# Optimization experiments

Hardware: AMD Instinct MI355X
Metric: run time of the kernel (lower is better)

Reference implementation:

```python
import jax, jax.numpy as jnp
import numpy as np

D_MODEL = 512
N_HEADS = 8
D_KV = 64
INNER = N_HEADS * D_KV
NUM_BUCKETS = 32
MAX_DISTANCE = 128
LN_EPS = 1e-6


def _relative_position_bucket(rel, num_buckets=NUM_BUCKETS, max_distance=MAX_DISTANCE):
    # bidirectional T5 bucketing
    nb = num_buckets // 2
    buckets = (rel > 0).astype(jnp.int32) * nb
    rel = jnp.abs(rel)
    max_exact = nb // 2
    is_small = rel < max_exact
    relf = jnp.maximum(rel.astype(jnp.float32), 1.0)  # guard log(0)
    large = max_exact + (
        jnp.log(relf / max_exact) / np.log(max_distance / max_exact) * (nb - max_exact)
    ).astype(jnp.int32)
    large = jnp.minimum(large, nb - 1)
    return buckets + jnp.where(is_small, rel, large)


def t5_layer_norm(x, weight, eps=LN_EPS):
    # T5 LayerNorm: no mean subtraction, no bias
    var = jnp.mean(jnp.square(x), axis=-1, keepdims=True)
    return x * jax.lax.rsqrt(var + eps) * weight


def compute_position_bias(rel_bias_table, q_len, k_len):
    ctx = jnp.arange(q_len)[:, None]
    mem = jnp.arange(k_len)[None, :]
    buckets = _relative_position_bucket(mem - ctx)  # [q, k]
    bias = rel_bias_table[buckets]                  # [q, k, H]
    return jnp.transpose(bias, (2, 0, 1))[None]     # [1, H, q, k]


def setup_inputs() -> dict:
    key = jax.random.key(0)
    ks = jax.random.split(key, 8)
    N, S = 8, 2048
    s = 1.0 / np.sqrt(D_MODEL)
    return {
        "hidden_states": jax.random.normal(ks[0], (N, S, D_MODEL), jnp.float32),
        "ln_weight": jnp.ones((D_MODEL,), jnp.float32),
        "wq": jax.random.normal(ks[1], (D_MODEL, INNER), jnp.float32) * s,
        "wk": jax.random.normal(ks[2], (D_MODEL, INNER), jnp.float32) * s,
        "wv": jax.random.normal(ks[3], (D_MODEL, INNER), jnp.float32) * s,
        "wo": jax.random.normal(ks[4], (INNER, D_MODEL), jnp.float32) * s,
        "rel_bias_table": jax.random.normal(ks[5], (NUM_BUCKETS, N_HEADS), jnp.float32) * 0.1,
        "seq_idx2graph_idx": jax.random.randint(ks[6], (8,), 0, 8, jnp.int64) if jax.config.jax_enable_x64 else jax.random.randint(ks[6], (8,), 0, 8, jnp.int32),
    }


def reference(hidden_states, ln_weight, wq, wk, wv, wo, rel_bias_table, seq_idx2graph_idx):
    N, S, _ = hidden_states.shape
    normed = t5_layer_norm(hidden_states, ln_weight)

    # T5Attention (no 1/sqrt(d) scaling in T5)
    q = jnp.einsum("nsd,de->nse", normed, wq).reshape(N, S, N_HEADS, D_KV)
    k = jnp.einsum("nsd,de->nse", normed, wk).reshape(N, S, N_HEADS, D_KV)
    v = jnp.einsum("nsd,de->nse", normed, wv).reshape(N, S, N_HEADS, D_KV)

    position_bias = compute_position_bias(rel_bias_table, S, S)  # [1,H,S,S]
    scores = jnp.einsum("nqhd,nkhd->nhqk", q, k) + position_bias
    attn = jax.nn.softmax(scores, axis=-1)
    ctx = jnp.einsum("nhqk,nkhd->nqhd", attn, v).reshape(N, S, INNER)
    attn_out = jnp.einsum("nse,ed->nsd", ctx, wo)

    # residual (dropout is identity in eval)
    hidden = hidden_states + attn_out
    remain_node_idx = jnp.arange(seq_idx2graph_idx.shape[0])
    return hidden, position_bias, remain_node_idx
```

## Files before the change

### kernel.cpp

```cpp
#include <hip/hip_runtime.h>
#include <hip/hip_bf16.h>
#include <math.h>

typedef __bf16 bf16;
typedef bf16 bf16x8 __attribute__((ext_vector_type(8)));
typedef bf16 bf16x4 __attribute__((ext_vector_type(4)));
typedef float f32x4 __attribute__((ext_vector_type(4)));
typedef float f32x16 __attribute__((ext_vector_type(16)));

#define MFMA16(a, b, c) __builtin_amdgcn_mfma_f32_16x16x32_bf16(a, b, c, 0, 0, 0)
#define MFMA32(a, b, c) __builtin_amdgcn_mfma_f32_32x32x16_bf16(a, b, c, 0, 0, 0)
#define LOG2E 1.4426950408889634f
#define NEG_SHIFT -40.0f

__device__ __forceinline__ void glds16(const bf16* g, bf16* l) {
  __builtin_amdgcn_global_load_lds(
      (const __attribute__((address_space(1))) void*)g,
      (__attribute__((address_space(3))) void*)l, 16, 0, 0);
}

__device__ inline unsigned pkbf(float a, float b) {
  union { bf16 h; unsigned short u; } ca, cb;
  ca.h = (bf16)a;
  cb.h = (bf16)b;
  return (unsigned)ca.u | ((unsigned)cb.u << 16);
}

__device__ inline float t5bias(const float* __restrict__ table, int h, int x) {
  if (x > 4094) return 0.f;
  int rel = x - 2047;
  int bucket = (rel > 0) ? 16 : 0;
  int ar = rel < 0 ? -rel : rel;
  int v;
  if (ar < 8) {
    v = ar;
  } else {
    double tt = log((double)ar / 8.0) / log(16.0) * 8.0;
    int lg = 8 + (int)tt;
    v = lg < 15 ? lg : 15;
  }
  return table[(bucket + v) * 8 + h];
}

__global__ __launch_bounds__(256) void prep_kernel(
    const float* __restrict__ hidden, const float* __restrict__ ln_w,
    const float* __restrict__ wq, const float* __restrict__ wk,
    const float* __restrict__ wv, const float* __restrict__ wo,
    const float* __restrict__ table, bf16* __restrict__ normed,
    float* __restrict__ lut, float4* __restrict__ lutq,
    float* __restrict__ out_remain, bf16* __restrict__ wt_qkv,
    bf16* __restrict__ wt_o) {
  __shared__ float tile[32][33];
  int bid = blockIdx.x;
  int t = threadIdx.x;
  if (bid < 4096) {
    int row = bid * 4 + (t >> 6);
    int lane = t & 63;
    const float4* xr = (const float4*)(hidden + (size_t)row * 512);
    float4 a = xr[lane];
    float4 b = xr[lane + 64];
    float s = a.x * a.x + a.y * a.y + a.z * a.z + a.w * a.w +
              b.x * b.x + b.y * b.y + b.z * b.z + b.w * b.w;
#pragma unroll
    for (int off = 32; off > 0; off >>= 1) s += __shfl_down(s, off, 64);
    float tot = __shfl(s, 0, 64);
    float rscale = rsqrtf(tot * (1.0f / 512.0f) + 1e-6f);
    float4 w0 = *(const float4*)(ln_w + 4 * lane);
    float4 w1 = *(const float4*)(ln_w + 256 + 4 * lane);
    bf16x4 o0, o1;
    o0[0] = (bf16)(a.x * rscale * w0.x);
    o0[1] = (bf16)(a.y * rscale * w0.y);
    o0[2] = (bf16)(a.z * rscale * w0.z);
    o0[3] = (bf16)(a.w * rscale * w0.w);
    o1[0] = (bf16)(b.x * rscale * w1.x);
    o1[1] = (bf16)(b.y * rscale * w1.y);
    o1[2] = (bf16)(b.z * rscale * w1.z);
    o1[3] = (bf16)(b.w * rscale * w1.w);
    *(bf16x4*)(normed + (size_t)row * 512 + 4 * lane) = o0;
    *(bf16x4*)(normed + (size_t)row * 512 + 256 + 4 * lane) = o1;
  } else if (bid < 4224) {
    int i = (bid - 4096) * 256 + t;
    int h = i >> 12;
    int d = i & 4095;
    lut[(size_t)h * 4096 + d] = t5bias(table, h, d);
    if (i < 8) out_remain[i] = (float)i;
  } else if (bid < 5248) {
    int bid2 = bid - 4224;
    int mat = bid2 >> 8;
    int rem = bid2 & 255;
    int e0 = (rem & 15) * 32;
    int k0 = (rem >> 4) * 32;
    int tx = t & 31, ty = t >> 5;
    const float* W = (mat == 0) ? wq : (mat == 1) ? wk : (mat == 2) ? wv : wo;
#pragma unroll
    for (int j = 0; j < 32; j += 8)
      tile[ty + j][tx] = W[(size_t)(k0 + ty + j) * 512 + e0 + tx];
    __syncthreads();
    bf16* dst = (mat < 3) ? (wt_qkv + (size_t)mat * 512 * 512) : wt_o;
#pragma unroll
    for (int j = 0; j < 32; j += 8)
      dst[(size_t)(e0 + ty + j) * 512 + k0 + tx] = (bf16)tile[tx][ty + j];
  } else {
    int i = (bid - 5248) * 256 + t;
    int h = i >> 12;
    int d = i & 4095;
    float4 o;
    o.x = t5bias(table, h, d);
    o.y = t5bias(table, h, d + 1);
    o.z = t5bias(table, h, d + 2);
    o.w = t5bias(table, h, d + 3);
    lutq[(size_t)h * 4096 + d] = o;
  }
}

__global__ __launch_bounds__(256) void qkv_gemm(
    const bf16* __restrict__ normed, const bf16* __restrict__ wt,
    bf16* __restrict__ qb, bf16* __restrict__ kb, bf16* __restrict__ vtb) {
  __shared__ __align__(16) char smem[19456];
  bf16* As = (bf16*)smem;
  bf16* Bs = (bf16*)(smem + 8192);
  int t = threadIdx.x;
  int wave = t >> 6, lane = t & 63;
  int quad = lane >> 4, lc = lane & 15;
  int wm = wave >> 1, wn = wave & 1;
  int m0 = blockIdx.x * 128, n0 = blockIdx.y * 128;

  f32x4 acc[4][4];
#pragma unroll
  for (int i = 0; i < 4; i++)
#pragma unroll
    for (int j = 0; j < 4; j++) acc[i][j] = (f32x4){0.f, 0.f, 0.f, 0.f};

  int rw = lane >> 2;
  int c8 = (lane & 3) * 8;
  const bf16* gA = normed + (size_t)(m0 + wave * 32 + rw) * 512 + c8;
  const bf16* gB = wt + (size_t)(n0 + wave * 32 + rw) * 512 + c8;
  bf16* lA = As + wave * 1024;
  bf16* lB = Bs + wave * 1024;

  for (int kt = 0; kt < 16; ++kt) {
    int k0 = kt * 32;
    __syncthreads();
    glds16(gA + k0, lA);
    glds16(gA + 16 * 512 + k0, lA + 512);
    glds16(gB + k0, lB);
    glds16(gB + 16 * 512 + k0, lB + 512);
    __syncthreads();
    bf16x8 af[4], bfr[4];
#pragma unroll
    for (int i = 0; i < 4; i++)
      af[i] = *(const bf16x8*)&As[(wm * 64 + i * 16 + lc) * 32 + quad * 8];
#pragma unroll
    for (int j = 0; j < 4; j++)
      bfr[j] = *(const bf16x8*)&Bs[(wn * 64 + j * 16 + lc) * 32 + quad * 8];
#pragma unroll
    for (int i = 0; i < 4; i++)
#pragma unroll
      for (int j = 0; j < 4; j++)
        acc[i][j] = MFMA16(af[i], bfr[j], acc[i][j]);
  }

  __syncthreads();
  int mat = n0 >> 9;
  int e_base = (n0 & 511) + wn * 64;
  int hh = e_base >> 6;
  int grow0 = m0 + wm * 64;
  int nbi = grow0 >> 11, sbase = grow0 & 2047;

  if (mat == 2) {
    bf16* dv = vtb + ((size_t)(nbi * 8 + hh) * 64) * 2048;
#pragma unroll
    for (int i = 0; i < 4; i++) {
      int s = sbase + i * 16 + quad * 4;
#pragma unroll
      for (int j = 0; j < 4; j++) {
        int d = j * 16 + lc;
        bf16x4 o4;
#pragma unroll
        for (int r = 0; r < 4; r++) o4[r] = (bf16)acc[i][j][r];
        *(bf16x4*)(dv + (size_t)d * 2048 + s) = o4;
      }
    }
  } else {
    bf16* dst0 = (mat == 0) ? qb : kb;
    bf16* dst = dst0 + (((size_t)nbi * 8 + hh) * 2048 + sbase) * 64;
    bf16* Cw = (bf16*)smem + wave * 2432;
#pragma unroll
    for (int p = 0; p < 2; ++p) {
#pragma unroll
      for (int i2 = 0; i2 < 2; ++i2) {
#pragma unroll
        for (int j = 0; j < 4; ++j)
#pragma unroll
          for (int r = 0; r < 4; ++r)
            Cw[(i2 * 16 + quad * 4 + r) * 76 + j * 16 + lc] =
                (bf16)acc[2 * p + i2][j][r];
      }
#pragma unroll
      for (int c = 0; c < 4; ++c) {
        bf16x8 vch =
            *(const bf16x8*)&Cw[(c * 8 + (lane >> 3)) * 76 + (lane & 7) * 8];
        *(bf16x8*)(dst + (size_t)(p * 32 + c * 8 + (lane >> 3)) * 64 +
                   (lane & 7) * 8) = vch;
      }
    }
  }
}

__global__ __launch_bounds__(256, 3) void attn_bias_kernel(
    const bf16* __restrict__ qg, const bf16* __restrict__ kg,
    const bf16* __restrict__ vtg, const float4* __restrict__ lutq,
    const float* __restrict__ lutg, bf16* __restrict__ ctx,
    float* __restrict__ bias_out) {
  __shared__ bf16 Ks[64][72];
  __shared__ bf16 Vs[64][72];
  int t = threadIdx.x;

  if (blockIdx.x >= 1024) {
    size_t i = (((size_t)blockIdx.x - 1024) * 256 + t) * 4;
    int h = (int)(i >> 22);
    int q = (int)((i >> 11) & 2047);
    int k = (int)(i & 2047);
    const float* lh = lutg + (size_t)h * 4096 + (2047 - q);
    float4 v = {lh[k], lh[k + 1], lh[k + 2], lh[k + 3]};
    *(float4*)(bias_out + i) = v;
    return;
  }

  int id = blockIdx.x;
  int xcd = id & 7, slot = id >> 3;
  int bh = xcd * 8 + (slot >> 4);
  int qt = slot & 15;
  int n = bh >> 3, h = bh & 7;
  int q0 = qt * 128;

  int wave = t >> 6, lane = t & 63;
  int l31 = lane & 31, hi = lane >> 5;
  int q = q0 + wave * 32 + l31;

  const float4* bq = lutq + (size_t)h * 4096;
  int cbase = 2047 + 4 * hi - q;

  const bf16* qp = qg + ((size_t)bh * 2048 + q) * 64;
  bf16x8 Qf[4];
#pragma unroll
  for (int c = 0; c < 4; c++) Qf[c] = *(const bf16x8*)(qp + c * 16 + hi * 8);

  f32x16 O[2];
#pragma unroll
  for (int i = 0; i < 2; i++)
#pragma unroll
    for (int e = 0; e < 16; e++) O[i][e] = 0.f;
  float lsum0 = 0.f, lsum1 = 0.f;

  int srow = t >> 2, scol = (t & 3) * 16;
  const bf16* kp = kg + (size_t)bh * 2048 * 64;
  const bf16* vp = vtg + (size_t)bh * 64 * 2048;

  bf16x8 kv0 = *(const bf16x8*)(kp + (size_t)srow * 64 + scol);
  bf16x8 kv1 = *(const bf16x8*)(kp + (size_t)srow * 64 + scol + 8);
  bf16x8 vv0 = *(const bf16x8*)(vp + (size_t)srow * 2048 + scol);
  bf16x8 vv1 = *(const bf16x8*)(vp + (size_t)srow * 2048 + scol + 8);

  for (int kt = 0; kt < 32; ++kt) {
    int kr0 = kt * 64;
    __syncthreads();
    *(bf16x8*)&Ks[srow][scol] = kv0;
    *(bf16x8*)&Ks[srow][scol + 8] = kv1;
    *(bf16x8*)&Vs[srow][scol] = vv0;
    *(bf16x8*)&Vs[srow][scol + 8] = vv1;
    __syncthreads();

    f32x16 st[2];
#pragma unroll
    for (int mi = 0; mi < 2; mi++)
#pragma unroll
      for (int g = 0; g < 4; g++) {
        float4 b4 = bq[cbase + kr0 + mi * 32 + 8 * g];
        st[mi][4 * g + 0] = b4.x;
        st[mi][4 * g + 1] = b4.y;
        st[mi][4 * g + 2] = b4.z;
        st[mi][4 * g + 3] = b4.w;
      }

    if (kt + 1 < 32) {
      int kn = kr0 + 64;
      kv0 = *(const bf16x8*)(kp + (size_t)(kn + srow) * 64 + scol);
      kv1 = *(const bf16x8*)(kp + (size_t)(kn + srow) * 64 + scol + 8);
      vv0 = *(const bf16x8*)(vp + (size_t)srow * 2048 + kn + scol);
      vv1 = *(const bf16x8*)(vp + (size_t)srow * 2048 + kn + scol + 8);
    }

#pragma unroll
    for (int mi = 0; mi < 2; mi++) {
#pragma unroll
      for (int c = 0; c < 4; c++) {
        bf16x8 kf = *(const bf16x8*)&Ks[mi * 32 + l31][c * 16 + hi * 8];
        st[mi] = MFMA32(kf, Qf[c], st[mi]);
      }
      unsigned D[8], X[8];
#pragma unroll
      for (int g = 0; g < 4; g++) {
#pragma unroll
        for (int e = 0; e < 4; e++) {
          float p = __builtin_amdgcn_exp2f(fmaf(st[mi][4 * g + e], LOG2E, NEG_SHIFT));
          st[mi][4 * g + e] = p;
          if (e & 1) lsum1 += p; else lsum0 += p;
        }
        D[2 * g] = pkbf(st[mi][4 * g + 0], st[mi][4 * g + 1]);
        D[2 * g + 1] = pkbf(st[mi][4 * g + 2], st[mi][4 * g + 3]);
      }
#pragma unroll
      for (int tt = 0; tt < 8; tt++) X[tt] = __shfl_xor(D[tt], 32, 64);

#pragma unroll
      for (int kk = 0; kk < 2; kk++) {
        int kc = 2 * mi + kk;
        int b = 4 * kk;
        unsigned f0 = hi ? X[b + 2] : D[b + 0];
        unsigned f1 = hi ? X[b + 3] : D[b + 1];
        unsigned f2 = hi ? D[b + 2] : X[b + 0];
        unsigned f3 = hi ? D[b + 3] : X[b + 1];
        union { uint4 u; bf16x8 v; } cv;
        cv.u = make_uint4(f0, f1, f2, f3);
        bf16x8 pf = cv.v;
#pragma unroll
        for (int md = 0; md < 2; md++) {
          bf16x8 vf = *(const bf16x8*)&Vs[md * 32 + l31][kc * 16 + hi * 8];
          O[md] = MFMA32(vf, pf, O[md]);
        }
      }
    }
  }

  float l_run = lsum0 + lsum1;
  l_run += __shfl_xor(l_run, 32, 64);
  float inv = 1.0f / l_run;
  bf16* cp = ctx + ((size_t)n * 2048 + q) * 512 + h * 64;
#pragma unroll
  for (int md = 0; md < 2; md++)
#pragma unroll
    for (int g = 0; g < 4; g++) {
      bf16x4 o4;
#pragma unroll
      for (int e = 0; e < 4; e++) o4[e] = (bf16)(O[md][4 * g + e] * inv);
      *(bf16x4*)(cp + md * 32 + 8 * g + hi * 4) = o4;
    }
}

__global__ __launch_bounds__(256) void oproj_gemm(
    const bf16* __restrict__ ctx, const bf16* __restrict__ wt_o,
    const float* __restrict__ hidden, float* __restrict__ out) {
  __shared__ __align__(16) char smem[16384];
  bf16* As = (bf16*)smem;
  bf16* Bs = (bf16*)(smem + 8192);
  int t = threadIdx.x;
  int wave = t >> 6, lane = t & 63;
  int quad = lane >> 4, lc = lane & 15;
  int wm = wave >> 1, wn = wave & 1;
  int m0 = blockIdx.x * 128, n0 = blockIdx.y * 128;

  f32x4 acc[4][4];
#pragma unroll
  for (int i = 0; i < 4; i++)
#pragma unroll
    for (int j = 0; j < 4; j++) acc[i][j] = (f32x4){0.f, 0.f, 0.f, 0.f};

  int rw = lane >> 2;
  int c8 = (lane & 3) * 8;
  const bf16* gA = ctx + (size_t)(m0 + wave * 32 + rw) * 512 + c8;
  const bf16* gB = wt_o + (size_t)(n0 + wave * 32 + rw) * 512 + c8;
  bf16* lA = As + wave * 1024;
  bf16* lB = Bs + wave * 1024;

  for (int kt = 0; kt < 16; ++kt) {
    int k0 = kt * 32;
    __syncthreads();
    glds16(gA + k0, lA);
    glds16(gA + 16 * 512 + k0, lA + 512);
    glds16(gB + k0, lB);
    glds16(gB + 16 * 512 + k0, lB + 512);
    __syncthreads();
    bf16x8 af[4], bfr[4];
#pragma unroll
    for (int i = 0; i < 4; i++)
      af[i] = *(const bf16x8*)&As[(wm * 64 + i * 16 + lc) * 32 + quad * 8];
#pragma unroll
    for (int j = 0; j < 4; j++)
      bfr[j] = *(const bf16x8*)&Bs[(wn * 64 + j * 16 + lc) * 32 + quad * 8];
#pragma unroll
    for (int i = 0; i < 4; i++)
#pragma unroll
      for (int j = 0; j < 4; j++)
        acc[i][j] = MFMA16(af[i], bfr[j], acc[i][j]);
  }

#pragma unroll
  for (int i = 0; i < 4; i++) {
#pragma unroll
    for (int j = 0; j < 4; j++) {
#pragma unroll
      for (int r = 0; r < 4; r++) {
        int grow = m0 + wm * 64 + i * 16 + quad * 4 + r;
        int gcol = n0 + wn * 64 + j * 16 + lc;
        size_t idx = (size_t)grow * 512 + gcol;
        out[idx] = acc[i][j][r] + hidden[idx];
      }
    }
  }
}

extern "C" void kernel_launch(void* const* d_in, const int* in_sizes, int n_in,
                              void* d_out, int out_size, void* d_ws, size_t ws_size,
                              hipStream_t stream) {
  const float* hidden = (const float*)d_in[0];
  const float* ln_w = (const float*)d_in[1];
  const float* wq = (const float*)d_in[2];
  const float* wk = (const float*)d_in[3];
  const float* wv = (const float*)d_in[4];
  const float* wo = (const float*)d_in[5];
  const float* table = (const float*)d_in[6];

  float* out_hidden = (float*)d_out;
  float* out_bias = out_hidden + (size_t)8 * 2048 * 512;
  float* out_remain = out_bias + (size_t)8 * 2048 * 2048;

  char* ws = (char*)d_ws;
  bf16* normed = (bf16*)(ws + 0);
  float* lut = (float*)(ws + 16777216);
  float4* lutq = (float4*)(ws + 16908288);
  bf16* wt_qkv = (bf16*)(ws + 17432576);
  bf16* wt_o = (bf16*)(ws + 19005440);
  bf16* qb = (bf16*)(ws + 19529728);
  bf16* kb = qb + (size_t)8 * 8 * 2048 * 64;
  bf16* vtb = kb + (size_t)8 * 8 * 2048 * 64;
  bf16* ctx = normed;

  prep_kernel<<<dim3(5376), dim3(256), 0, stream>>>(
      hidden, ln_w, wq, wk, wv, wo, table, normed, lut, lutq, out_remain,
      wt_qkv, wt_o);
  qkv_gemm<<<dim3(128, 12), dim3(256), 0, stream>>>(normed, wt_qkv, qb, kb, vtb);
  attn_bias_kernel<<<dim3(1024 + 32768), dim3(256), 0, stream>>>(
      qb, kb, vtb, lutq, lut, ctx, out_bias);
  oproj_gemm<<<dim3(128, 4), dim3(256), 0, stream>>>(ctx, wt_o, hidden, out_hidden);
}
```

Before: 358.4 us.

## Double-buffer attention K/V via async global-to-LDS loads with XOR swizzle

The attention kernel now stages K and V tiles directly into LDS with global_load_lds into two alternating buffers, so the next tile streams in while the current one is consumed. This replaces register staging and drops one barrier per iteration. Shared-memory rows are XOR-swizzled to avoid bank conflicts, and occupancy is raised to 4 blocks per SM. The QKV and output-projection GEMMs move to a 64-wide K tile with the same swizzled LDS layout, halving the number of barriers, at the cost of more LDS and tighter register limits.

```diff
diff --git a/kernel.cpp b/kernel.cpp
--- a/kernel.cpp
+++ b/kernel.cpp
@@ -116,9 +116,8 @@
 __global__ __launch_bounds__(256) void qkv_gemm(
     const bf16* __restrict__ normed, const bf16* __restrict__ wt,
     bf16* __restrict__ qb, bf16* __restrict__ kb, bf16* __restrict__ vtb) {
-  __shared__ __align__(16) char smem[19456];
-  bf16* As = (bf16*)smem;
-  bf16* Bs = (bf16*)(smem + 8192);
+  __shared__ __align__(16) bf16 As[128 * 64];
+  __shared__ __align__(16) bf16 Bs[128 * 64];
   int t = threadIdx.x;
   int wave = t >> 6, lane = t & 63;
   int quad = lane >> 4, lc = lane & 15;
@@ -131,33 +130,39 @@
 #pragma unroll
     for (int j = 0; j < 4; j++) acc[i][j] = (f32x4){0.f, 0.f, 0.f, 0.f};
 
-  int rw = lane >> 2;
-  int c8 = (lane & 3) * 8;
-  const bf16* gA = normed + (size_t)(m0 + wave * 32 + rw) * 512 + c8;
-  const bf16* gB = wt + (size_t)(n0 + wave * 32 + rw) * 512 + c8;
-  bf16* lA = As + wave * 1024;
-  bf16* lB = Bs + wave * 1024;
-
-  for (int kt = 0; kt < 16; ++kt) {
-    int k0 = kt * 32;
-    __syncthreads();
-    glds16(gA + k0, lA);
-    glds16(gA + 16 * 512 + k0, lA + 512);
-    glds16(gB + k0, lB);
-    glds16(gB + 16 * 512 + k0, lB + 512);
-    __syncthreads();
-    bf16x8 af[4], bfr[4];
-#pragma unroll
-    for (int i = 0; i < 4; i++)
-      af[i] = *(const bf16x8*)&As[(wm * 64 + i * 16 + lc) * 32 + quad * 8];
-#pragma unroll
-    for (int j = 0; j < 4; j++)
-      bfr[j] = *(const bf16x8*)&Bs[(wn * 64 + j * 16 + lc) * 32 + quad * 8];
-#pragma unroll
-    for (int i = 0; i < 4; i++)
+  int sw8 = (lane & 7) ^ ((lane >> 3) & 7);
+  const bf16* gA = normed + (size_t)(m0 + wave * 32 + (lane >> 3)) * 512 + sw8 * 8;
+  const bf16* gB = wt + (size_t)(n0 + wave * 32 + (lane >> 3)) * 512 + sw8 * 8;
+  bf16* lA = As + wave * 32 * 64;
+  bf16* lB = Bs + wave * 32 * 64;
+  int rx = lc & 7;
+
+  for (int kt = 0; kt < 8; ++kt) {
+    int k0 = kt * 64;
+    __syncthreads();
+#pragma unroll
+    for (int j = 0; j < 4; ++j) {
+      glds16(gA + (size_t)j * 8 * 512 + k0, lA + j * 8 * 64);
+      glds16(gB + (size_t)j * 8 * 512 + k0, lB + j * 8 * 64);
+    }
+    __syncthreads();
+#pragma unroll
+    for (int kc = 0; kc < 2; ++kc) {
+      bf16x8 af[4], bfr[4];
+#pragma unroll
+      for (int i = 0; i < 4; i++)
+        af[i] = *(const bf16x8*)&As[(wm * 64 + i * 16 + lc) * 64 +
+                                    (((kc * 4 + quad) ^ rx) * 8)];
 #pragma unroll
       for (int j = 0; j < 4; j++)
-        acc[i][j] = MFMA16(af[i], bfr[j], acc[i][j]);
+        bfr[j] = *(const bf16x8*)&Bs[(wn * 64 + j * 16 + lc) * 64 +
+                                     (((kc * 4 + quad) ^ rx) * 8)];
+#pragma unroll
+      for (int i = 0; i < 4; i++)
+#pragma unroll
+        for (int j = 0; j < 4; j++)
+          acc[i][j] = MFMA16(af[i], bfr[j], acc[i][j]);
+    }
   }
 
   __syncthreads();
@@ -184,7 +189,7 @@
   } else {
     bf16* dst0 = (mat == 0) ? qb : kb;
     bf16* dst = dst0 + (((size_t)nbi * 8 + hh) * 2048 + sbase) * 64;
-    bf16* Cw = (bf16*)smem + wave * 2432;
+    bf16* Cw = As + wave * 2432;
 #pragma unroll
     for (int p = 0; p < 2; ++p) {
 #pragma unroll
@@ -207,13 +212,12 @@
   }
 }
 
-__global__ __launch_bounds__(256, 3) void attn_bias_kernel(
+__global__ __launch_bounds__(256, 4) void attn_bias_kernel(
     const bf16* __restrict__ qg, const bf16* __restrict__ kg,
     const bf16* __restrict__ vtg, const float4* __restrict__ lutq,
     const float* __restrict__ lutg, bf16* __restrict__ ctx,
     float* __restrict__ bias_out) {
-  __shared__ bf16 Ks[64][72];
-  __shared__ bf16 Vs[64][72];
+  __shared__ __align__(16) bf16 KV[2][2][64 * 64];
   int t = threadIdx.x;
 
   if (blockIdx.x >= 1024) {
@@ -253,62 +257,66 @@
     for (int e = 0; e < 16; e++) O[i][e] = 0.f;
   float lsum0 = 0.f, lsum1 = 0.f;
 
-  int srow = t >> 2, scol = (t & 3) * 16;
-  const bf16* kp = kg + (size_t)bh * 2048 * 64;
-  const bf16* vp = vtg + (size_t)bh * 64 * 2048;
-
-  bf16x8 kv0 = *(const bf16x8*)(kp + (size_t)srow * 64 + scol);
-  bf16x8 kv1 = *(const bf16x8*)(kp + (size_t)srow * 64 + scol + 8);
-  bf16x8 vv0 = *(const bf16x8*)(vp + (size_t)srow * 2048 + scol);
-  bf16x8 vv1 = *(const bf16x8*)(vp + (size_t)srow * 2048 + scol + 8);
+  int sw8 = (lane & 7) ^ ((lane >> 3) & 7);
+  int rx = l31 & 7;
+  const bf16* kp = kg + ((size_t)bh * 2048 + wave * 16 + (lane >> 3)) * 64 + sw8 * 8;
+  const bf16* vp = vtg + ((size_t)bh * 64 + wave * 16 + (lane >> 3)) * 2048 + sw8 * 8;
+  bf16* lK0 = &KV[0][0][0] + (wave * 16) * 64;
+  bf16* lV0 = &KV[0][1][0] + (wave * 16) * 64;
+
+#pragma unroll
+  for (int j = 0; j < 2; ++j) {
+    glds16(kp + (size_t)j * 8 * 64, lK0 + j * 8 * 64);
+    glds16(vp + j * 8 * 2048, lV0 + j * 8 * 64);
+  }
 
   for (int kt = 0; kt < 32; ++kt) {
     int kr0 = kt * 64;
-    __syncthreads();
-    *(bf16x8*)&Ks[srow][scol] = kv0;
-    *(bf16x8*)&Ks[srow][scol + 8] = kv1;
-    *(bf16x8*)&Vs[srow][scol] = vv0;
-    *(bf16x8*)&Vs[srow][scol + 8] = vv1;
-    __syncthreads();
-
-    f32x16 st[2];
-#pragma unroll
-    for (int mi = 0; mi < 2; mi++)
+    int cur = kt & 1;
+    __syncthreads();
+    if (kt + 1 < 32) {
+      int nb = cur ^ 1;
+      const bf16* kpn = kp + (size_t)(kr0 + 64) * 64;
+      const bf16* vpn = vp + (kr0 + 64);
+      bf16* lKn = lK0 + nb * 2 * 4096;
+      bf16* lVn = lV0 + nb * 2 * 4096;
+#pragma unroll
+      for (int j = 0; j < 2; ++j) {
+        glds16(kpn + (size_t)j * 8 * 64, lKn + j * 8 * 64);
+        glds16(vpn + j * 8 * 2048, lVn + j * 8 * 64);
+      }
+    }
+    const bf16* Ks = &KV[cur][0][0];
+    const bf16* Vs = &KV[cur][1][0];
+
+#pragma unroll
+    for (int mi = 0; mi < 2; mi++) {
+      f32x16 st;
 #pragma unroll
       for (int g = 0; g < 4; g++) {
         float4 b4 = bq[cbase + kr0 + mi * 32 + 8 * g];
-        st[mi][4 * g + 0] = b4.x;
-        st[mi][4 * g + 1] = b4.y;
-        st[mi][4 * g + 2] = b4.z;
-        st[mi][4 * g + 3] = b4.w;
-      }
-
-    if (kt + 1 < 32) {
-      int kn = kr0 + 64;
-      kv0 = *(const bf16x8*)(kp + (size_t)(kn + srow) * 64 + scol);
-      kv1 = *(const bf16x8*)(kp + (size_t)(kn + srow) * 64 + scol + 8);
-      vv0 = *(const bf16x8*)(vp + (size_t)srow * 2048 + kn + scol);
-      vv1 = *(const bf16x8*)(vp + (size_t)srow * 2048 + kn + scol + 8);
-    }
-
-#pragma unroll
-    for (int mi = 0; mi < 2; mi++) {
+        st[4 * g + 0] = b4.x;
+        st[4 * g + 1] = b4.y;
+        st[4 * g + 2] = b4.z;
+        st[4 * g + 3] = b4.w;
+      }
 #pragma unroll
       for (int c = 0; c < 4; c++) {
-        bf16x8 kf = *(const bf16x8*)&Ks[mi * 32 + l31][c * 16 + hi * 8];
-        st[mi] = MFMA32(kf, Qf[c], st[mi]);
+        bf16x8 kf = *(const bf16x8*)&Ks[(mi * 32 + l31) * 64 +
+                                        (((c * 2 + hi) ^ rx) * 8)];
+        st = MFMA32(kf, Qf[c], st);
       }
       unsigned D[8], X[8];
 #pragma unroll
       for (int g = 0; g < 4; g++) {
 #pragma unroll
         for (int e = 0; e < 4; e++) {
-          float p = __builtin_amdgcn_exp2f(fmaf(st[mi][4 * g + e], LOG2E, NEG_SHIFT));
-          st[mi][4 * g + e] = p;
+          float p = __builtin_amdgcn_exp2f(fmaf(st[4 * g + e], LOG2E, NEG_SHIFT));
+          st[4 * g + e] = p;
           if (e & 1) lsum1 += p; else lsum0 += p;
         }
-        D[2 * g] = pkbf(st[mi][4 * g + 0], st[mi][4 * g + 1]);
-        D[2 * g + 1] = pkbf(st[mi][4 * g + 2], st[mi][4 * g + 3]);
+        D[2 * g] = pkbf(st[4 * g + 0], st[4 * g + 1]);
+        D[2 * g + 1] = pkbf(st[4 * g + 2], st[4 * g + 3]);
       }
 #pragma unroll
       for (int tt = 0; tt < 8; tt++) X[tt] = __shfl_xor(D[tt], 32, 64);
@@ -326,7 +334,8 @@
         bf16x8 pf = cv.v;
 #pragma unroll
         for (int md = 0; md < 2; md++) {
-          bf16x8 vf = *(const bf16x8*)&Vs[md * 32 + l31][kc * 16 + hi * 8];
+          bf16x8 vf = *(const bf16x8*)&Vs[(md * 32 + l31) * 64 +
+                                          (((kc * 2 + hi) ^ rx) * 8)];
           O[md] = MFMA32(vf, pf, O[md]);
         }
       }
@@ -351,9 +360,8 @@
 __global__ __launch_bounds__(256) void oproj_gemm(
     const bf16* __restrict__ ctx, const bf16* __restrict__ wt_o,
     const float* __restrict__ hidden, float* __restrict__ out) {
-  __shared__ __align__(16) char smem[16384];
-  bf16* As = (bf16*)smem;
-  bf16* Bs = (bf16*)(smem + 8192);
+  __shared__ __align__(16) bf16 As[128 * 64];
+  __shared__ __align__(16) bf16 Bs[128 * 64];
   int t = threadIdx.x;
   int wave = t >> 6, lane = t & 63;
   int quad = lane >> 4, lc = lane & 15;
@@ -366,33 +374,39 @@
 #pragma unroll
     for (int j = 0; j < 4; j++) acc[i][j] = (f32x4){0.f, 0.f, 0.f, 0.f};
 
-  int rw = lane >> 2;
-  int c8 = (lane & 3) * 8;
-  const bf16* gA = ctx + (size_t)(m0 + wave * 32 + rw) * 512 + c8;
-  const bf16* gB = wt_o + (size_t)(n0 + wave * 32 + rw) * 512 + c8;
-  bf16* lA = As + wave * 1024;
-  bf16* lB = Bs + wave * 1024;
-
-  for (int kt = 0; kt < 16; ++kt) {
-    int k0 = kt * 32;
-    __syncthreads();
-    glds16(gA + k0, lA);
-    glds16(gA + 16 * 512 + k0, lA + 512);
-    glds16(gB + k0, lB);
-    glds16(gB + 16 * 512 + k0, lB + 512);
-    __syncthreads();
-    bf16x8 af[4], bfr[4];
-#pragma unroll
-    for (int i = 0; i < 4; i++)
-      af[i] = *(const bf16x8*)&As[(wm * 64 + i * 16 + lc) * 32 + quad * 8];
-#pragma unroll
-    for (int j = 0; j < 4; j++)
-      bfr[j] = *(const bf16x8*)&Bs[(wn * 64 + j * 16 + lc) * 32 + quad * 8];
-#pragma unroll
-    for (int i = 0; i < 4; i++)
+  int sw8 = (lane & 7) ^ ((lane >> 3) & 7);
+  const bf16* gA = ctx + (size_t)(m0 + wave * 32 + (lane >> 3)) * 512 + sw8 * 8;
+  const bf16* gB = wt_o + (size_t)(n0 + wave * 32 + (lane >> 3)) * 512 + sw8 * 8;
+  bf16* lA = As + wave * 32 * 64;
+  bf16* lB = Bs + wave * 32 * 64;
+  int rx = lc & 7;
+
+  for (int kt = 0; kt < 8; ++kt) {
+    int k0 = kt * 64;
+    __syncthreads();
+#pragma unroll
+    for (int j = 0; j < 4; ++j) {
+      glds16(gA + (size_t)j * 8 * 512 + k0, lA + j * 8 * 64);
+      glds16(gB + (size_t)j * 8 * 512 + k0, lB + j * 8 * 64);
+    }
+    __syncthreads();
+#pragma unroll
+    for (int kc = 0; kc < 2; ++kc) {
+      bf16x8 af[4], bfr[4];
+#pragma unroll
+      for (int i = 0; i < 4; i++)
+        af[i] = *(const bf16x8*)&As[(wm * 64 + i * 16 + lc) * 64 +
+                                    (((kc * 4 + quad) ^ rx) * 8)];
 #pragma unroll
       for (int j = 0; j < 4; j++)
-        acc[i][j] = MFMA16(af[i], bfr[j], acc[i][j]);
+        bfr[j] = *(const bf16x8*)&Bs[(wn * 64 + j * 16 + lc) * 64 +
+                                     (((kc * 4 + quad) ^ rx) * 8)];
+#pragma unroll
+      for (int i = 0; i < 4; i++)
+#pragma unroll
+        for (int j = 0; j < 4; j++)
+          acc[i][j] = MFMA16(af[i], bfr[j], acc[i][j]);
+    }
   }
 
 #pragma unroll
```

New measurement: 358.9 us. Within noise of the previous version (+0.1%).
